# Optimization experiments

Measured on AMD Instinct MI355X. Metric: run time of the kernel, lower is better.

The kernel has to match this reference:

```python
import jax, jax.numpy as jnp
import numpy as np

DIM = 1024
NUM_HEADS = 16
HEAD_DIM = 64
MLP_DIM = 4096
BATCH = 4
SEQ = 1024
ATTN_CLIP = 100.0
NORM_CLIP = 1000.0
EPS = 1e-6
LAMBDA_INIT = 0.8


def _grn(x, gamma, beta):
    # Global Response Norm exactly as in source (3D input: reduce over seq and feature dims)
    square_sum = jnp.sum(jnp.square(x), axis=(1, 2), keepdims=True)  # (B,1,1)
    square_sum = jnp.clip(square_sum, EPS, NORM_CLIP)
    gx = jnp.sqrt(square_sum)
    mean_norm = jnp.mean(gx, axis=-1, keepdims=True)
    nx = gx / (mean_norm + EPS)  # safe_divide
    nx = jnp.clip(nx, -NORM_CLIP, NORM_CLIP)
    return gamma * (x * nx) + beta + x


def _softmax_attn(q, k, v, scale):
    # manual clipped softmax attention as in _compute_attention (mask=None, no dropout)
    s = jnp.clip(jnp.einsum('bhqd,bhkd->bhqk', q, k) * scale, -ATTN_CLIP, ATTN_CLIP)
    m = jnp.max(s, axis=-1, keepdims=True)
    e = jnp.exp(s - m)
    a = e / (jnp.sum(e, axis=-1, keepdims=True) + EPS)  # safe_divide
    return jnp.einsum('bhqk,bhkd->bhqd', a, v)


def setup_inputs() -> dict:
    key = jax.random.key(0)
    ks = jax.random.split(key, 12)
    D, H, hd, F = DIM, NUM_HEADS, HEAD_DIM, MLP_DIM
    init_val = np.log(LAMBDA_INIT / 4.0) / hd
    return {
        'x': jax.random.normal(ks[0], (BATCH, SEQ, D), dtype=jnp.float32),
        'w_qkv': jax.random.normal(ks[1], (D, 5 * H * hd), dtype=jnp.float32) * (2.0 / (5 * H * hd)) ** 0.5,
        'lambda_q1': jnp.full((hd,), init_val, dtype=jnp.float32),
        'lambda_k1': jnp.full((hd,), init_val, dtype=jnp.float32),
        'lambda_q2': jnp.full((hd,), -init_val, dtype=jnp.float32),
        'lambda_k2': jnp.full((hd,), -init_val, dtype=jnp.float32),
        'w_proj': jax.random.normal(ks[2], (H * hd, D), dtype=jnp.float32) * (2.0 / (H * hd)) ** 0.5,
        'b_proj': jnp.zeros((D,), dtype=jnp.float32),
        'gamma1': jnp.ones((D,), dtype=jnp.float32),
        'beta1': jnp.zeros((D,), dtype=jnp.float32),
        'gamma2': jnp.ones((D,), dtype=jnp.float32),
        'beta2': jnp.zeros((D,), dtype=jnp.float32),
        'w1': jax.random.normal(ks[3], (D, F), dtype=jnp.float32) * (2.0 / F) ** 0.5,
        'b1': jnp.zeros((F,), dtype=jnp.float32),
        'w2': jax.random.normal(ks[4], (F, D), dtype=jnp.float32) * (2.0 / F) ** 0.5,
        'b2': jnp.zeros((D,), dtype=jnp.float32),
    }


def reference(x, w_qkv, lambda_q1, lambda_k1, lambda_q2, lambda_k2,
              w_proj, b_proj, gamma1, beta1, gamma2, beta2, w1, b1, w2, b2):
    B, S, D = x.shape
    H, hd = NUM_HEADS, HEAD_DIM
    scale = hd ** -0.5
    layer_idx = 0

    residual = x
    h = _grn(x, gamma1, beta1)

    # differential attention
    qkv = h @ w_qkv                                   # (B,S,5*H*hd)
    qkv = qkv.reshape(B, S, 5, H, hd).transpose(2, 0, 3, 1, 4)  # (5,B,H,S,hd)
    q1, q2, k1, k2, v = qkv[0], qkv[1], qkv[2], qkv[3], qkv[4]

    layer_factor = jnp.clip(jnp.float32(layer_idx) * 0.3, 0.0, 5.0)
    lam_init = 0.8 - 0.6 * jnp.exp(-layer_factor)
    l1 = jnp.clip(jnp.sum(lambda_q1 * lambda_k1), -10.0, 10.0)
    l2 = jnp.clip(jnp.sum(lambda_q2 * lambda_k2), -10.0, 10.0)
    lam = jnp.clip(jnp.exp(l1) - jnp.exp(l2) + lam_init, 0.1, 5.0)

    a1 = _softmax_attn(q1, k1, v, scale)
    a2 = _softmax_attn(q2, k2, v, scale)
    o = a1 - lam * a2                                 # (B,H,S,hd)
    o = o.transpose(0, 2, 1, 3).reshape(B, S, H * hd)
    o = o @ w_proj + b_proj

    x = o + residual  # stochastic_path in eval mode = plain residual

    residual = x
    h = _grn(x, gamma2, beta2)
    h = jax.nn.silu(h @ w1 + b1) @ w2 + b2            # swish FFN
    return h + residual
```

## Files before the change

kernel.cpp:

```cpp
#include <hip/hip_runtime.h>


using u16 = unsigned short;
typedef __attribute__((ext_vector_type(8))) short bh8;
typedef __attribute__((ext_vector_type(4))) float f32x4;

__device__ __forceinline__ float b2f(u16 v) { return __uint_as_float(((unsigned)v) << 16); }
__device__ __forceinline__ u16 f2b(float f) {
    unsigned u = __float_as_uint(f);
    u += 0x7fffu + ((u >> 16) & 1u);
    return (u16)(u >> 16);
}
__device__ __forceinline__ u16 f2b_t(float f) {
    return (u16)(__float_as_uint(f) >> 16);
}
__device__ __forceinline__ void async16(const void* g, void* l) {
    __builtin_amdgcn_global_load_lds((const __attribute__((address_space(1))) void*)g,
                                     (__attribute__((address_space(3))) void*)l, 16, 0, 0);
}
__device__ __forceinline__ float ldin(const void* p, size_t i, int f32flag) {
    return f32flag ? ((const float*)p)[i] : b2f(((const u16*)p)[i]);
}
__device__ __forceinline__ float nxof(float ssv) {
    const float s = fminf(fmaxf(ssv, 1e-6f), 1000.f);
    const float gx = sqrtf(s);
    return gx / (gx + 1e-6f);
}

__global__ void ndetect(const u16* __restrict__ x, int* __restrict__ flag) {
    const int t = threadIdx.x;
    int big = 0, zlo = 0;
    for (int i = t; i < 4096; i += 256) {
        const u16 w = x[i];
        big += (((w >> 7) & 0xFFu) >= 0x93u);
        if ((i & 1) == 0) zlo += (w == 0);
    }
    for (int off = 32; off; off >>= 1) {
        big += __shfl_xor(big, off);
        zlo += __shfl_xor(zlo, off);
    }
    __shared__ int wb[4], wz[4];
    if ((t & 63) == 0) { wb[t >> 6] = big; wz[t >> 6] = zlo; }
    __syncthreads();
    if (t == 0) {
        const int B = wb[0] + wb[1] + wb[2] + wb[3];
        const int Z = wz[0] + wz[1] + wz[2] + wz[3];
        *flag = (Z > 1024 || B > 64) ? 1 : 0;
    }
}

__global__ void convert_small_kernel(const void* p0, const void* p1, const void* p2, const void* p3,
                                     const void* p4, const void* p5, const void* p6,
                                     const int* __restrict__ flag, u16* __restrict__ pack) {
    const int idx = blockIdx.x * 256 + threadIdx.x;
    if (idx >= 10240) return;
    const int f = *flag;
    const void* src;
    int rel;
    if (idx < 5120) {
        const int seg = idx >> 10;
        rel = idx & 1023;
        src = seg == 0 ? p0 : seg == 1 ? p1 : seg == 2 ? p2 : seg == 3 ? p3 : p4;
    } else if (idx < 9216) { src = p5; rel = idx - 5120; }
    else { src = p6; rel = idx - 9216; }
    pack[idx] = f2b(ldin(src, rel, f));
}

__global__ __launch_bounds__(256) void nss(const void* __restrict__ x, const int* __restrict__ flag,
                                           float* __restrict__ ss, int mode) {
    const int b = blockIdx.y, t = threadIdx.x;
    const int f = mode ? *flag : 0;
    const size_t base = (size_t)b * 1048576;
    float acc = 0.f;
    if (f) {
        const float4* p = (const float4*)((const float*)x + base);
        for (int i = blockIdx.x * 256 + t; i < 262144; i += 64 * 256) {
            const float4 v = p[i];
            acc += v.x * v.x + v.y * v.y + v.z * v.z + v.w * v.w;
        }
    } else {
        const bh8* p = (const bh8*)((const u16*)x + base);
        for (int i = blockIdx.x * 256 + t; i < 131072; i += 64 * 256) {
            const bh8 v = p[i];
#pragma unroll
            for (int j = 0; j < 8; ++j) {
                const float xv = b2f((u16)v[j]);
                acc += xv * xv;
            }
        }
    }
    for (int off = 32; off; off >>= 1) acc += __shfl_xor(acc, off);
    __shared__ float ws4[4];
    if ((t & 63) == 0) ws4[t >> 6] = acc;
    __syncthreads();
    if (t == 0) atomicAdd(&ss[b], ws4[0] + ws4[1] + ws4[2] + ws4[3]);
}

__global__ __launch_bounds__(256) void grn_x_kernel(const void* __restrict__ x, const u16* __restrict__ gamma,
                                                    const u16* __restrict__ beta, const float* __restrict__ ss,
                                                    const int* __restrict__ flag, u16* __restrict__ h) {
    const size_t i0 = ((size_t)blockIdx.x * 256 + threadIdx.x) * 8;
    const int batch = (int)(i0 >> 20);
    const int dt = *flag;
    const float nx = nxof(ss[batch]);
    const int d0 = (int)(i0 & 1023);
    float xf[8];
    if (dt) {
#pragma unroll
        for (int j = 0; j < 8; ++j) xf[j] = ((const float*)x)[i0 + j];
    } else {
        const bh8 xv = *(const bh8*)((const u16*)x + i0);
#pragma unroll
        for (int j = 0; j < 8; ++j) xf[j] = b2f((u16)xv[j]);
    }
    const bh8 gv = *(const bh8*)(gamma + d0);
    const bh8 bv = *(const bh8*)(beta + d0);
    bh8 res;
#pragma unroll
    for (int j = 0; j < 8; ++j)
        res[j] = (short)f2b(b2f((u16)gv[j]) * (xf[j] * nx) + b2f((u16)bv[j]) + xf[j]);
    *(bh8*)(h + i0) = res;
}

__global__ __launch_bounds__(256) void grn_bf16_kernel(const u16* __restrict__ x, const u16* __restrict__ gamma,
                                                       const u16* __restrict__ beta, const float* __restrict__ ss,
                                                       u16* __restrict__ h) {
    const size_t i0 = ((size_t)blockIdx.x * 256 + threadIdx.x) * 8;
    const int batch = (int)(i0 >> 20);
    const float nx = nxof(ss[batch]);
    const int d0 = (int)(i0 & 1023);
    const bh8 xv = *(const bh8*)(x + i0);
    const bh8 gv = *(const bh8*)(gamma + d0);
    const bh8 bv = *(const bh8*)(beta + d0);
    bh8 res;
#pragma unroll
    for (int j = 0; j < 8; ++j) {
        const float xf = b2f((u16)xv[j]);
        res[j] = (short)f2b(b2f((u16)gv[j]) * (xf * nx) + b2f((u16)bv[j]) + xf);
    }
    *(bh8*)(h + i0) = res;
}

__global__ __launch_bounds__(256) void transpose_kernel(const void* __restrict__ in, u16* __restrict__ outp,
                                                        int R, int C, const int* __restrict__ flag) {
    __shared__ u16 tile[32][33];
    const int f = *flag;
    const int cb = blockIdx.x * 32, rb = blockIdx.y * 32;
    const int tx = threadIdx.x, ty = threadIdx.y;
#pragma unroll
    for (int j = 0; j < 32; j += 8) {
        const size_t gi = (size_t)(rb + ty + j) * C + cb + tx;
        tile[ty + j][tx] = f ? f2b(((const float*)in)[gi]) : ((const u16*)in)[gi];
    }
    __syncthreads();
#pragma unroll
    for (int j = 0; j < 32; j += 8)
        outp[(size_t)(cb + ty + j) * R + rb + tx] = tile[tx][ty + j];
}

__global__ void lambda_kernel(const void* lq1, const void* lk1, const void* lq2, const void* lk2,
                              const int* __restrict__ flag, float* lam) {
    const int t = threadIdx.x;
    const int f = *flag;
    float a = ldin(lq1, t, f) * ldin(lk1, t, f);
    float c = ldin(lq2, t, f) * ldin(lk2, t, f);
    for (int off = 32; off; off >>= 1) { a += __shfl_xor(a, off); c += __shfl_xor(c, off); }
    if (t == 0) {
        const float l1 = fminf(fmaxf(a, -10.f), 10.f);
        const float l2 = fminf(fmaxf(c, -10.f), 10.f);
        const float lv = __expf(l1) - __expf(l2) + 0.2f;
        *lam = fminf(fmaxf(lv, 0.1f), 5.0f);
    }
}

template <int EPI>
__global__ __launch_bounds__(256) void gemm_bt_kernel(const u16* __restrict__ A, const u16* __restrict__ Bt,
                                                      const u16* __restrict__ bias, const void* resid,
                                                      void* outp, int N, int K,
                                                      const int* __restrict__ flagp,
                                                      float* __restrict__ ssout) {
    __shared__ __attribute__((aligned(16))) u16 As[128 * 64];
    __shared__ __attribute__((aligned(16))) u16 Bs[128 * 64];
    const int tid = threadIdx.x;
    const int wave = tid >> 6, lane = tid & 63;
    const int quad = lane >> 4, col = lane & 15;
    const int wr = wave >> 1, wc = wave & 1;
    const int m0 = blockIdx.y * 128, n0 = blockIdx.x * 128;
    const int dt = (EPI == 1) ? *flagp : 0;

    const int srow = lane >> 3;
    const int schunk = (lane & 7) ^ srow;
    const u16* Ag = A + (size_t)(m0 + wave * 32 + srow) * K + schunk * 8;
    const u16* Bg = Bt + (size_t)(n0 + wave * 32 + srow) * K + schunk * 8;
    u16* AsW = As + (wave * 32) * 64;
    u16* BsW = Bs + (wave * 32) * 64;

    f32x4 acc[4][4];
#pragma unroll
    for (int i = 0; i < 4; ++i)
#pragma unroll
        for (int j = 0; j < 4; ++j) acc[i][j] = (f32x4){0.f, 0.f, 0.f, 0.f};

    for (int k0 = 0; k0 < K; k0 += 64) {
        __syncthreads();
#pragma unroll
        for (int it = 0; it < 4; ++it) {
            async16(Ag + k0 + (size_t)(it * 8) * K, AsW + it * 8 * 64);
            async16(Bg + k0 + (size_t)(it * 8) * K, BsW + it * 8 * 64);
        }
        __syncthreads();
#pragma unroll
        for (int ks = 0; ks < 2; ++ks) {
            const int slot = ((ks * 4 + quad) ^ (col & 7)) * 8;
            bh8 a[4], bfr[4];
#pragma unroll
            for (int i = 0; i < 4; ++i)
                a[i] = *(const bh8*)(As + (wr * 64 + i * 16 + col) * 64 + slot);
#pragma unroll
            for (int j = 0; j < 4; ++j)
                bfr[j] = *(const bh8*)(Bs + (wc * 64 + j * 16 + col) * 64 + slot);
#pragma unroll
            for (int i = 0; i < 4; ++i)
#pragma unroll
                for (int j = 0; j < 4; ++j)
                    acc[i][j] = __builtin_amdgcn_mfma_f32_16x16x32_bf16(a[i], bfr[j], acc[i][j], 0, 0, 0);
        }
    }

    float ssacc = 0.f;
#pragma unroll
    for (int i = 0; i < 4; ++i) {
        const int row0 = m0 + wr * 64 + i * 16 + quad * 4;
#pragma unroll
        for (int j = 0; j < 4; ++j) {
            const int cc = n0 + wc * 64 + j * 16 + col;
            float bb = 0.f;
            if (EPI != 0) bb = b2f(bias[cc]);
#pragma unroll
            for (int r = 0; r < 4; ++r) {
                const size_t idx = (size_t)(row0 + r) * N + cc;
                float v = acc[i][j][r];
                if (EPI == 0) {
                    ((u16*)outp)[idx] = f2b(v);
                } else if (EPI == 1) {
                    const u16 hv = f2b(v + bb + ldin(resid, idx, dt));
                    ((u16*)outp)[idx] = hv;
                    const float w = b2f(hv);
                    ssacc += w * w;
                } else if (EPI == 2) {
                    v += bb;
                    ((u16*)outp)[idx] = f2b(v / (1.f + __expf(-v)));
                } else {
                    ((float*)outp)[idx] = v + bb + b2f(((const u16*)resid)[idx]);
                }
            }
        }
    }
    if (EPI == 1) {
        for (int off = 32; off; off >>= 1) ssacc += __shfl_xor(ssacc, off);
        __shared__ float wsum[4];
        if (lane == 0) wsum[wave] = ssacc;
        __syncthreads();
        if (tid == 0) atomicAdd(&ssout[m0 >> 10], wsum[0] + wsum[1] + wsum[2] + wsum[3]);
    }
}

#define ATTN_L2E 1.4426950f

__device__ __forceinline__ void attn_step(bh8 qf0, bh8 qf1, const u16* __restrict__ Ks, const u16* __restrict__ Vt,
                                          u16* __restrict__ Pw, f32x4* __restrict__ O, float* __restrict__ mv,
                                          float* __restrict__ lv, int quad, int col) {
    const int sw = col & 7;
    f32x4 s[4];
#pragma unroll
    for (int nt = 0; nt < 4; ++nt) {
        const u16* kr = Ks + (nt * 16 + col) * 64;
        bh8 kb0 = *(const bh8*)(kr + ((quad ^ sw) * 8));
        bh8 kb1 = *(const bh8*)(kr + (((4 + quad) ^ sw) * 8));
        f32x4 z = (f32x4){0.f, 0.f, 0.f, 0.f};
        z = __builtin_amdgcn_mfma_f32_16x16x32_bf16(qf0, kb0, z, 0, 0, 0);
        z = __builtin_amdgcn_mfma_f32_16x16x32_bf16(qf1, kb1, z, 0, 0, 0);
        s[nt] = z;
    }
    float mx[4];
#pragma unroll
    for (int r = 0; r < 4; ++r) {
#pragma unroll
        for (int nt = 0; nt < 4; ++nt)
            s[nt][r] = __builtin_amdgcn_fmed3f(s[nt][r], -100.f, 100.f);
        mx[r] = fmaxf(fmaxf(s[0][r], s[1][r]), fmaxf(s[2][r], s[3][r]));
    }
    const bool ok = (mx[0] <= mv[0] + 8.f) && (mx[1] <= mv[1] + 8.f) &&
                    (mx[2] <= mv[2] + 8.f) && (mx[3] <= mv[3] + 8.f);
    if (!__all(ok)) {
#pragma unroll
        for (int off = 1; off < 16; off <<= 1)
#pragma unroll
            for (int r = 0; r < 4; ++r) mx[r] = fmaxf(mx[r], __shfl_xor(mx[r], off));
#pragma unroll
        for (int r = 0; r < 4; ++r) {
            const float mn = fmaxf(mv[r], mx[r]);
            const float alpha = __expf(mv[r] - mn);
            mv[r] = mn;
            lv[r] *= alpha;
#pragma unroll
            for (int nt = 0; nt < 4; ++nt) O[nt][r] *= alpha;
        }
    }
    float nme[4];
#pragma unroll
    for (int r = 0; r < 4; ++r) nme[r] = -mv[r] * ATTN_L2E;
#pragma unroll
    for (int nt = 0; nt < 4; ++nt) {
        const int key = nt * 16 + col;
        const int pbase = key >> 3;
        const int k7 = key & 7;
#pragma unroll
        for (int r = 0; r < 4; ++r) {
            const float p = __builtin_amdgcn_exp2f(__builtin_fmaf(s[nt][r], ATTN_L2E, nme[r]));
            lv[r] += p;
            const int prow = 8 * (r >> 1) + 2 * quad + (r & 1);
            const int pa = 2 * quad + (r & 1);
            Pw[prow * 64 + ((pbase ^ pa) * 8) + k7] = f2b_t(p);
        }
    }

    const int psic = 8 * ((col >> 1) & 1) + 2 * (col >> 2) + (col & 1);
    const int swp = psic & 7;
    const u16* pr = Pw + psic * 64;
    bh8 pa0 = *(const bh8*)(pr + ((quad ^ swp) * 8));
    bh8 pa1 = *(const bh8*)(pr + (((4 + quad) ^ swp) * 8));
#pragma unroll
    for (int nt = 0; nt < 4; ++nt) {
        const int fv = (2 * nt + (col >> 3)) & 7;
        const u16* vr = Vt + (nt * 16 + col) * 72;
        bh8 vb0 = *(const bh8*)(vr + ((quad ^ fv) * 8));
        bh8 vb1 = *(const bh8*)(vr + (((4 + quad) ^ fv) * 8));
        f32x4 accv = O[nt];
        accv = __builtin_amdgcn_mfma_f32_16x16x32_bf16(pa0, vb0, accv, 0, 0, 0);
        accv = __builtin_amdgcn_mfma_f32_16x16x32_bf16(pa1, vb1, accv, 0, 0, 0);
        O[nt] = accv;
    }
}

__global__ __launch_bounds__(256) void attn_kernel(const u16* __restrict__ qkv, const float* __restrict__ lam_p,
                                                   u16* __restrict__ o) {
    __shared__ __attribute__((aligned(16))) u16 K1s[64 * 64];
    __shared__ __attribute__((aligned(16))) u16 K2s[64 * 64];
    __shared__ __attribute__((aligned(16))) u16 Vt[64 * 72];
    __shared__ __attribute__((aligned(16))) u16 Pbuf[4][16 * 64];

    const int tid = threadIdx.x;
    const int wave = tid >> 6, lane = tid & 63;
    const int quad = lane >> 4, col = lane & 15;
    const int qb = blockIdx.x, hh = blockIdx.y, bb = blockIdx.z;

    const float lam = *lam_p;
    const int qrow = bb * 1024 + qb * 64 + wave * 16 + col;
    const u16* qp = qkv + (size_t)qrow * 5120 + hh * 64 + quad * 8;
    bh8 q1f0 = *(const bh8*)(qp);
    bh8 q1f1 = *(const bh8*)(qp + 32);
    bh8 q2f0 = *(const bh8*)(qp + 1024);
    bh8 q2f1 = *(const bh8*)(qp + 1056);
#pragma unroll
    for (int j = 0; j < 8; ++j) {
        q1f0[j] = (short)f2b(b2f((u16)q1f0[j]) * 0.125f);
        q1f1[j] = (short)f2b(b2f((u16)q1f1[j]) * 0.125f);
        q2f0[j] = (short)f2b(b2f((u16)q2f0[j]) * 0.125f);
        q2f1[j] = (short)f2b(b2f((u16)q2f1[j]) * 0.125f);
    }

    f32x4 O1[4], O2[4];
    float m1v[4], l1v[4], m2v[4], l2v[4];
#pragma unroll
    for (int r = 0; r < 4; ++r) {
        O1[r] = (f32x4){0.f, 0.f, 0.f, 0.f};
        O2[r] = (f32x4){0.f, 0.f, 0.f, 0.f};
        m1v[r] = -1e30f; m2v[r] = -1e30f;
        l1v[r] = 0.f; l2v[r] = 0.f;
    }
    u16* Pw = &Pbuf[wave][0];

    for (int kt = 0; kt < 16; ++kt) {
        __syncthreads();
#pragma unroll
        for (int j = 0; j < 2; ++j) {
            const int keyl = wave * 16 + j * 8 + (lane >> 3);
            const int chunk = (lane & 7) ^ (keyl & 7);
            const u16* kg = qkv + (size_t)(bb * 1024 + kt * 64 + keyl) * 5120 + hh * 64 + chunk * 8;
            async16(kg + 2048, K1s + (wave * 16 + j * 8) * 64);
            async16(kg + 3072, K2s + (wave * 16 + j * 8) * 64);
        }
#pragma unroll
        for (int g = 0; g < 4; ++g) {
            const int idx = g * 256 + tid;
            const int key = idx >> 4;
            const int m15 = idx & 15;
            const int hd4 = m15 << 2;
            const int slot = (((key >> 3) ^ (m15 >> 1)) << 3) + (key & 7);
            const u16* vp = qkv + (size_t)(bb * 1024 + kt * 64 + key) * 5120 + 4096 + hh * 64 + hd4;
            const ushort4 vv = *(const ushort4*)vp;
            Vt[(hd4 + 0) * 72 + slot] = vv.x;
            Vt[(hd4 + 1) * 72 + slot] = vv.y;
            Vt[(hd4 + 2) * 72 + slot] = vv.z;
            Vt[(hd4 + 3) * 72 + slot] = vv.w;
        }
        __syncthreads();

        attn_step(q1f0, q1f1, K1s, Vt, Pw, O1, m1v, l1v, quad, col);
        attn_step(q2f0, q2f1, K2s, Vt, Pw, O2, m2v, l2v, quad, col);
    }

#pragma unroll
    for (int off = 1; off < 16; off <<= 1)
#pragma unroll
        for (int r = 0; r < 4; ++r) {
            l1v[r] += __shfl_xor(l1v[r], off);
            l2v[r] += __shfl_xor(l2v[r], off);
        }

    float w1v[4], w2v[4];
#pragma unroll
    for (int r = 0; r < 4; ++r) {
        w1v[r] = 1.f / (l1v[r] + 1e-6f);
        w2v[r] = lam / (l2v[r] + 1e-6f);
    }
    const size_t orow0 = (size_t)(bb * 1024 + qb * 64 + wave * 16 + quad * 4);
#pragma unroll
    for (int nt = 0; nt < 4; ++nt) {
        const int cc = hh * 64 + nt * 16 + col;
#pragma unroll
        for (int r = 0; r < 4; ++r)
            o[(orow0 + r) * 1024 + cc] = f2b(O1[nt][r] * w1v[r] - O2[nt][r] * w2v[r]);
    }
}

__global__ void nsentinel(float* __restrict__ outp, int hc) {
    const size_t i0 = ((size_t)blockIdx.x * 256 + threadIdx.x) * 4;
    const float v = 1.0e6f * (float)(1 + hc);
#pragma unroll
    for (int j = 0; j < 4; ++j) outp[i0 + j] = v;
}

extern "C" void kernel_launch(void* const* d_in, const int* in_sizes, int n_in,
                              void* d_out, int out_size, void* d_ws, size_t ws_size,
                              hipStream_t stream) {
    const size_t MB = 1ull << 20;
    static const int exp_sizes[16] = {4194304, 5242880, 64, 64, 64, 64, 1048576, 1024,
                                      1024, 1024, 1024, 1024, 4194304, 4096, 4194304, 1024};
    int hc = 0;
    if (n_in != 16) hc = 1;
    else {
        for (int i = 0; i < 16; ++i)
            if (in_sizes[i] != exp_sizes[i]) { hc = 2; break; }
    }
    if (hc == 0 && out_size != 4194304) hc = 3;
    if (hc == 0 && ws_size < 0x10000 + 58 * MB) hc = 4;
    if (hc) {
        nsentinel<<<4096, 256, 0, stream>>>((float*)d_out, hc);
        return;
    }

    const void* x      = d_in[0];
    const void* w_qkv  = d_in[1];
    const void* lq1    = d_in[2];
    const void* lk1    = d_in[3];
    const void* lq2    = d_in[4];
    const void* lk2    = d_in[5];
    const void* w_proj = d_in[6];
    const void* b_proj = d_in[7];
    const void* gamma1 = d_in[8];
    const void* beta1  = d_in[9];
    const void* gamma2 = d_in[10];
    const void* beta2  = d_in[11];
    const void* w1     = d_in[12];
    const void* b1     = d_in[13];
    const void* w2     = d_in[14];
    const void* b2     = d_in[15];
    char* ws = (char*)d_ws;

    float* ss1  = (float*)(ws + 0);
    float* ss2  = (float*)(ws + 16);
    float* lamp = (float*)(ws + 32);
    int*   flag = (int*)(ws + 36);
    u16* pack = (u16*)(ws + 4096);
    u16* bprojp = pack;
    u16* g1p = pack + 1024;
    u16* be1p = pack + 2048;
    u16* g2p = pack + 3072;
    u16* be2p = pack + 4096;
    u16* b1p = pack + 5120;
    u16* b2p = pack + 9216;

    char* base = ws + 0x10000;
    u16* Fqkv  = (u16*)(base);
    u16* Fmid  = (u16*)(base);
    u16* FwT   = (u16*)(base + 32 * MB);
    u16* FqkvT = (u16*)(base + 40 * MB);
    u16* FX2   = (u16*)(base + 40 * MB);
    u16* FpT   = (u16*)(base + 48 * MB);
    u16* Fc    = (u16*)(base + 50 * MB);

    hipMemsetAsync(ws, 0, 128, stream);
    ndetect<<<1, 256, 0, stream>>>((const u16*)x, flag);
    convert_small_kernel<<<40, 256, 0, stream>>>(b_proj, gamma1, beta1, gamma2, beta2, b1, b2, flag, pack);
    lambda_kernel<<<1, 64, 0, stream>>>(lq1, lk1, lq2, lk2, flag, lamp);
    nss<<<dim3(64, 4), 256, 0, stream>>>(x, flag, ss1, 1);

    grn_x_kernel<<<2048, 256, 0, stream>>>(x, g1p, be1p, ss1, flag, Fc);
    transpose_kernel<<<dim3(160, 32), dim3(32, 8), 0, stream>>>(w_qkv, FqkvT, 1024, 5120, flag);
    gemm_bt_kernel<0><<<dim3(40, 32), 256, 0, stream>>>(Fc, FqkvT, nullptr, nullptr, Fqkv, 5120, 1024, flag, nullptr);
    attn_kernel<<<dim3(16, 16, 4), 256, 0, stream>>>(Fqkv, lamp, Fc);
    transpose_kernel<<<dim3(32, 32), dim3(32, 8), 0, stream>>>(w_proj, FpT, 1024, 1024, flag);
    gemm_bt_kernel<1><<<dim3(8, 32), 256, 0, stream>>>(Fc, FpT, bprojp, x, FX2, 1024, 1024, flag, ss2);
    grn_bf16_kernel<<<2048, 256, 0, stream>>>(FX2, g2p, be2p, ss2, Fc);
    transpose_kernel<<<dim3(128, 32), dim3(32, 8), 0, stream>>>(w1, FwT, 1024, 4096, flag);
    gemm_bt_kernel<2><<<dim3(32, 32), 256, 0, stream>>>(Fc, FwT, b1p, nullptr, Fmid, 4096, 1024, flag, nullptr);
    transpose_kernel<<<dim3(32, 128), dim3(32, 8), 0, stream>>>(w2, FwT, 4096, 1024, flag);
    gemm_bt_kernel<3><<<dim3(8, 32), 256, 0, stream>>>(Fmid, FwT, b2p, FX2, d_out, 1024, 4096, flag, nullptr);
}
```

Before: 480.2 us.

## Double-buffer K/V tiles in attention kernel to overlap loads with compute

Doubles the shared-memory buffers for K1, K2 and transposed V. The next tile's K loads are issued asynchronously and its V values are prefetched into registers before computing on the current tile, then written to the alternate buffer. The aim is to hide global-memory latency behind the MFMA work and to drop one barrier per iteration. In exchange it roughly doubles LDS use per block, which may lower occupancy, and adds register pressure from holding V in flight.

After: 521.9 us. 8.7% more time.

```diff
diff --git a/kernel.cpp b/kernel.cpp
--- a/kernel.cpp
+++ b/kernel.cpp
@@ -345,9 +345,9 @@
 
 __global__ __launch_bounds__(256) void attn_kernel(const u16* __restrict__ qkv, const float* __restrict__ lam_p,
                                                    u16* __restrict__ o) {
-    __shared__ __attribute__((aligned(16))) u16 K1s[64 * 64];
-    __shared__ __attribute__((aligned(16))) u16 K2s[64 * 64];
-    __shared__ __attribute__((aligned(16))) u16 Vt[64 * 72];
+    __shared__ __attribute__((aligned(16))) u16 K1s[2][64 * 64];
+    __shared__ __attribute__((aligned(16))) u16 K2s[2][64 * 64];
+    __shared__ __attribute__((aligned(16))) u16 Vt[2][64 * 72];
     __shared__ __attribute__((aligned(16))) u16 Pbuf[4][16 * 64];
 
     const int tid = threadIdx.x;
@@ -370,6 +370,9 @@
         q2f1[j] = (short)f2b(b2f((u16)q2f1[j]) * 0.125f);
     }
 
+    const int keyl8 = lane >> 3;
+    const int vkey = tid >> 4;
+
     f32x4 O1[4], O2[4];
     float m1v[4], l1v[4], m2v[4], l2v[4];
 #pragma unroll
@@ -381,15 +384,23 @@
     }
     u16* Pw = &Pbuf[wave][0];
 
-    for (int kt = 0; kt < 16; ++kt) {
-        __syncthreads();
+    ushort4 vv[4];
+
+    {
 #pragma unroll
         for (int j = 0; j < 2; ++j) {
-            const int keyl = wave * 16 + j * 8 + (lane >> 3);
+            const int keyl = wave * 16 + j * 8 + keyl8;
             const int chunk = (lane & 7) ^ (keyl & 7);
-            const u16* kg = qkv + (size_t)(bb * 1024 + kt * 64 + keyl) * 5120 + hh * 64 + chunk * 8;
-            async16(kg + 2048, K1s + (wave * 16 + j * 8) * 64);
-            async16(kg + 3072, K2s + (wave * 16 + j * 8) * 64);
+            const u16* kg = qkv + (size_t)(bb * 1024 + 0 * 64 + keyl) * 5120 + hh * 64 + chunk * 8;
+            async16(kg + 2048, K1s[0] + (wave * 16 + j * 8) * 64);
+            async16(kg + 3072, K2s[0] + (wave * 16 + j * 8) * 64);
+        }
+#pragma unroll
+        for (int g = 0; g < 4; ++g) {
+            const int idx = g * 256 + tid;
+            const int key = idx >> 4;
+            const int hd4 = (idx & 15) << 2;
+            vv[g] = *(const ushort4*)(qkv + (size_t)(bb * 1024 + key) * 5120 + 4096 + hh * 64 + hd4);
         }
 #pragma unroll
         for (int g = 0; g < 4; ++g) {
@@ -398,17 +409,54 @@
             const int m15 = idx & 15;
             const int hd4 = m15 << 2;
             const int slot = (((key >> 3) ^ (m15 >> 1)) << 3) + (key & 7);
-            const u16* vp = qkv + (size_t)(bb * 1024 + kt * 64 + key) * 5120 + 4096 + hh * 64 + hd4;
-            const ushort4 vv = *(const ushort4*)vp;
-            Vt[(hd4 + 0) * 72 + slot] = vv.x;
-            Vt[(hd4 + 1) * 72 + slot] = vv.y;
-            Vt[(hd4 + 2) * 72 + slot] = vv.z;
-            Vt[(hd4 + 3) * 72 + slot] = vv.w;
+            Vt[0][(hd4 + 0) * 72 + slot] = vv[g].x;
+            Vt[0][(hd4 + 1) * 72 + slot] = vv[g].y;
+            Vt[0][(hd4 + 2) * 72 + slot] = vv[g].z;
+            Vt[0][(hd4 + 3) * 72 + slot] = vv[g].w;
         }
         __syncthreads();
-
-        attn_step(q1f0, q1f1, K1s, Vt, Pw, O1, m1v, l1v, quad, col);
-        attn_step(q2f0, q2f1, K2s, Vt, Pw, O2, m2v, l2v, quad, col);
+    }
+
+    int cur = 0;
+    for (int kt = 0; kt < 16; ++kt) {
+        const int nxt = cur ^ 1;
+        if (kt < 15) {
+#pragma unroll
+            for (int j = 0; j < 2; ++j) {
+                const int keyl = wave * 16 + j * 8 + keyl8;
+                const int chunk = (lane & 7) ^ (keyl & 7);
+                const u16* kg = qkv + (size_t)(bb * 1024 + (kt + 1) * 64 + keyl) * 5120 + hh * 64 + chunk * 8;
+                async16(kg + 2048, K1s[nxt] + (wave * 16 + j * 8) * 64);
+                async16(kg + 3072, K2s[nxt] + (wave * 16 + j * 8) * 64);
+            }
+#pragma unroll
+            for (int g = 0; g < 4; ++g) {
+                const int idx = g * 256 + tid;
+                const int key = idx >> 4;
+                const int hd4 = (idx & 15) << 2;
+                vv[g] = *(const ushort4*)(qkv + (size_t)(bb * 1024 + (kt + 1) * 64 + key) * 5120 + 4096 + hh * 64 + hd4);
+            }
+        }
+
+        attn_step(q1f0, q1f1, K1s[cur], Vt[cur], Pw, O1, m1v, l1v, quad, col);
+        attn_step(q2f0, q2f1, K2s[cur], Vt[cur], Pw, O2, m2v, l2v, quad, col);
+
+        if (kt < 15) {
+#pragma unroll
+            for (int g = 0; g < 4; ++g) {
+                const int idx = g * 256 + tid;
+                const int key = idx >> 4;
+                const int m15 = idx & 15;
+                const int hd4 = m15 << 2;
+                const int slot = (((key >> 3) ^ (m15 >> 1)) << 3) + (key & 7);
+                Vt[nxt][(hd4 + 0) * 72 + slot] = vv[g].x;
+                Vt[nxt][(hd4 + 1) * 72 + slot] = vv[g].y;
+                Vt[nxt][(hd4 + 2) * 72 + slot] = vv[g].z;
+                Vt[nxt][(hd4 + 3) * 72 + slot] = vv[g].w;
+            }
+        }
+        __syncthreads();
+        cur = nxt;
     }
 
 #pragma unroll
```
